# Kernel tuning notes

Hardware: AMD Instinct MI355X
Metric: run time of the kernel (lower is better)

Reference implementation:

```python
import jax, jax.numpy as jnp
import numpy as np

N_EMBD = 1024
N_HEAD = 16
HEAD_DIM = N_EMBD // N_HEAD
SCALE = 1.0 / np.sqrt(HEAD_DIM).astype(np.float32)


def setup_inputs() -> dict:
    key = jax.random.key(0)
    ks = jax.random.split(key, 9)
    B, T = 2, 2048
    std = 1.0 / np.sqrt(N_EMBD).astype(np.float32)
    x = jax.random.normal(ks[0], (B, T, N_EMBD), dtype=jnp.float32)
    Wq = jax.random.normal(ks[1], (N_EMBD, N_EMBD), dtype=jnp.float32) * std
    Wk = jax.random.normal(ks[2], (N_EMBD, N_EMBD), dtype=jnp.float32) * std
    Wv = jax.random.normal(ks[3], (N_EMBD, N_EMBD), dtype=jnp.float32) * std
    Wo = jax.random.normal(ks[4], (N_EMBD, N_EMBD), dtype=jnp.float32) * std
    bq = jax.random.normal(ks[5], (N_EMBD,), dtype=jnp.float32) * 0.01
    bk = jax.random.normal(ks[6], (N_EMBD,), dtype=jnp.float32) * 0.01
    bv = jax.random.normal(ks[7], (N_EMBD,), dtype=jnp.float32) * 0.01
    bo = jax.random.normal(ks[8], (N_EMBD,), dtype=jnp.float32) * 0.01
    return {"x": x, "Wq": Wq, "bq": bq, "Wk": Wk, "bk": bk,
            "Wv": Wv, "bv": bv, "Wo": Wo, "bo": bo}


def reference(x, Wq, bq, Wk, bk, Wv, bv, Wo, bo):
    B, T, C = x.shape
    # project and split heads: (B, H, T, D)
    def heads(y):
        return y.reshape(B, T, N_HEAD, HEAD_DIM).transpose(0, 2, 1, 3)
    q = heads(x @ Wq.T + bq)
    k = heads(x @ Wk.T + bk)
    v = heads(x @ Wv.T + bv)
    # materialized causal attention (matches the torch module's math)
    att = jnp.einsum("bhqd,bhkd->bhqk", q, k) * SCALE
    causal = jnp.tril(jnp.ones((T, T), dtype=bool))
    att = jnp.where(causal, att, -jnp.inf)
    att = jax.nn.softmax(att, axis=-1)
    out = jnp.einsum("bhqk,bhkd->bhqd", att, v)
    out = out.transpose(0, 2, 1, 3).reshape(B, T, C)
    return out @ Wo.T + bo
```

## Files before the change

kernel.cpp:

```cpp
#include <hip/hip_runtime.h>
#include <stdint.h>

typedef unsigned short u16;
typedef __attribute__((ext_vector_type(8))) short short8;
typedef __attribute__((ext_vector_type(4))) float f32x4;

__device__ __forceinline__ u16 f2bf(float f) {
  union { float f; unsigned int u; } c; c.f = f;
  return (u16)((c.u + 0x7FFFu + ((c.u >> 16) & 1u)) >> 16);
}

__device__ __forceinline__ float bf2f(u16 v) {
  union { unsigned int u; float f; } c; c.u = ((unsigned int)v) << 16;
  return c.f;
}

__device__ __forceinline__ f32x4 mfma16(short8 a, short8 b, f32x4 c) {
  return __builtin_amdgcn_mfma_f32_16x16x32_bf16(a, b, c, 0, 0, 0);
}

__device__ __forceinline__ void gl_lds16(const u16* g, u16* l) {
  __builtin_amdgcn_global_load_lds((const __attribute__((address_space(1))) void*)g,
                                   (__attribute__((address_space(3))) void*)l, 16, 0, 0);
}

__global__ __launch_bounds__(256) void cast_all(
    const float* __restrict__ x, const float* __restrict__ wq, const float* __restrict__ wk,
    const float* __restrict__ wv, const float* __restrict__ wo,
    u16* __restrict__ xb, u16* __restrict__ wqb, u16* __restrict__ wkb,
    u16* __restrict__ wvb, u16* __restrict__ wob) {
  int b = blockIdx.x;
  const float* src; u16* dst; int i;
  if (b < 4096)      { src = x;  dst = xb;  i = b * 256 + threadIdx.x; }
  else if (b < 5120) { src = wq; dst = wqb; i = (b - 4096) * 256 + threadIdx.x; }
  else if (b < 6144) { src = wk; dst = wkb; i = (b - 5120) * 256 + threadIdx.x; }
  else if (b < 7168) { src = wv; dst = wvb; i = (b - 6144) * 256 + threadIdx.x; }
  else               { src = wo; dst = wob; i = (b - 7168) * 256 + threadIdx.x; }
  float4 v = ((const float4*)src)[i];
  ushort4 o;
  o.x = f2bf(v.x); o.y = f2bf(v.y); o.z = f2bf(v.z); o.w = f2bf(v.w);
  ((ushort4*)dst)[i] = o;
}

__global__ __launch_bounds__(256) void qkv_gemm(
    const u16* __restrict__ xb, const u16* __restrict__ wqb, const u16* __restrict__ wkb,
    const u16* __restrict__ wvb, const float* __restrict__ bq, const float* __restrict__ bk,
    const float* __restrict__ bv, u16* __restrict__ Qb, u16* __restrict__ Kb,
    u16* __restrict__ VTb) {
  __shared__ __align__(16) u16 As[128 * 32];
  __shared__ __align__(16) u16 Bs[128 * 32];
  const int z = blockIdx.z;
  const u16* __restrict__ W = (z == 0) ? wqb : (z == 1) ? wkb : wvb;
  const float* __restrict__ bias = (z == 0) ? bq : (z == 1) ? bk : bv;
  const int m0 = blockIdx.y * 128, n0 = blockIdx.x * 128;
  const int tid = threadIdx.x, lane = tid & 63, wave = tid >> 6;
  const int wr = (wave >> 1) * 64, wc = (wave & 1) * 64;
  const int fr = lane & 15, fg = lane >> 4;
  const int lrow = lane >> 2, lcol = (lane & 3) * 8;

  const u16* ga = xb + (size_t)(m0 + wave * 16 + lrow) * 1024 + lcol;
  const u16* gb = W  + (size_t)(n0 + wave * 16 + lrow) * 1024 + lcol;
  u16* la = As + wave * 512;
  u16* lb = Bs + wave * 512;

  f32x4 acc[4][4] = {};

  for (int k0 = 0; k0 < 1024; k0 += 32) {
    gl_lds16(ga + k0, la);
    gl_lds16(ga + 64 * 1024 + k0, la + 2048);
    gl_lds16(gb + k0, lb);
    gl_lds16(gb + 64 * 1024 + k0, lb + 2048);
    __syncthreads();
    short8 a[4], b[4];
#pragma unroll
    for (int i = 0; i < 4; ++i) a[i] = *(const short8*)(As + (wr + i * 16 + fr) * 32 + fg * 8);
#pragma unroll
    for (int i = 0; i < 4; ++i) b[i] = *(const short8*)(Bs + (wc + i * 16 + fr) * 32 + fg * 8);
#pragma unroll
    for (int i = 0; i < 4; ++i)
#pragma unroll
      for (int j = 0; j < 4; ++j) acc[i][j] = mfma16(a[i], b[j], acc[i][j]);
    __syncthreads();
  }

  const float qsc = (z == 0) ? (0.125f * 1.44269504088896f) : 1.0f;
#pragma unroll
  for (int j = 0; j < 4; ++j) {
    const int col = n0 + wc + j * 16 + fr;
    const float bcol = bias[col];
    const int h = col >> 6, d = col & 63;
#pragma unroll
    for (int i = 0; i < 4; ++i) {
#pragma unroll
      for (int r = 0; r < 4; ++r) {
        const int m = m0 + wr + i * 16 + fg * 4 + r;
        const int bi = m >> 11, t = m & 2047;
        const u16 o = f2bf((acc[i][j][r] + bcol) * qsc);
        const size_t bse = (size_t)(bi * 16 + h) << 17;
        if (z == 0)      Qb[bse + (size_t)t * 64 + d] = o;
        else if (z == 1) Kb[bse + (size_t)t * 64 + d] = o;
        else             VTb[bse + (size_t)d * 2048 + t] = o;
      }
    }
  }
}

__global__ __launch_bounds__(256, 2) void attn_kernel(
    const u16* __restrict__ Qb, const u16* __restrict__ Kb, const u16* __restrict__ VTb,
    u16* __restrict__ aOb) {
  __shared__ __align__(16) char smem[4 * 64 * 72 * 2];
  __shared__ float Mll[4][4][64];
  u16* Ow = (u16*)smem;
  uint32_t* Pw = (uint32_t*)smem;
  const int id = blockIdx.x;
  const int bh = id & 31, j = 31 - (id >> 5);
  const int tid = threadIdx.x, lane = tid & 63, wave = tid >> 6;
  const int fr = lane & 15, fg = lane >> 4;
  const size_t base = (size_t)bh << 17;
  const int bi = bh >> 4, h = bh & 15;
  const int swz = (fr & 7) << 4;
  const int q0 = j * 64;

  short8 qf[4][2];
#pragma unroll
  for (int mi = 0; mi < 4; ++mi)
#pragma unroll
    for (int kk = 0; kk < 2; ++kk)
      qf[mi][kk] = *(const short8*)(Qb + base +
                    (size_t)(q0 + mi * 16 + fr) * 64 + kk * 32 + fg * 8);

  f32x4 oacc[4][4] = {};
  float lrun[4] = {0.f, 0.f, 0.f, 0.f};

  char* prow = (char*)&Pw[(wave * 16 + fr) * 32];

  for (int ti = wave; ti <= j; ti += 4) {
    const int t0 = ti * 64;
    const u16* kp = Kb + base + (size_t)(t0 + fr) * 64 + fg * 8;
    short8 kf[4][2];
#pragma unroll
    for (int ni = 0; ni < 4; ++ni) {
      kf[ni][0] = *(const short8*)(kp + ni * 1024);
      kf[ni][1] = *(const short8*)(kp + ni * 1024 + 32);
    }
    const u16* vp = VTb + base + (size_t)fr * 2048 + t0 + fg * 8;
    short8 vf[4][2];
#pragma unroll
    for (int ni = 0; ni < 4; ++ni) {
      vf[ni][0] = *(const short8*)(vp + (size_t)ni * 32768);
      vf[ni][1] = *(const short8*)(vp + (size_t)ni * 32768 + 32);
    }

#pragma unroll
    for (int mi = 0; mi < 4; ++mi) {
      f32x4 s[4] = {};
      __builtin_amdgcn_s_setprio(1);
#pragma unroll
      for (int ni = 0; ni < 4; ++ni) {
        s[ni] = mfma16(kf[ni][0], qf[mi][0], s[ni]);
        s[ni] = mfma16(kf[ni][1], qf[mi][1], s[ni]);
      }
      __builtin_amdgcn_s_setprio(0);

      if (ti == j) {
        const int rloc = mi * 16 + fr;
#pragma unroll
        for (int ni = 0; ni < 4; ++ni)
#pragma unroll
          for (int r = 0; r < 4; ++r)
            if (ni * 16 + fg * 4 + r > rloc) s[ni][r] = -1e30f;
      }

      float rs = 0.f;
#pragma unroll
      for (int ni = 0; ni < 4; ++ni)
#pragma unroll
        for (int r = 0; r < 4; ++r) {
          const float pv = exp2f(fminf(s[ni][r], 80.f));
          s[ni][r] = pv;
          rs += pv;
        }
      lrun[mi] += rs;

#pragma unroll
      for (int ni = 0; ni < 4; ++ni) {
        float a0 = s[ni][0], a1 = s[ni][1], a2 = s[ni][2], a3 = s[ni][3];
        uint32_t w0, w1;
        asm("v_cvt_pk_bf16_f32 %0, %1, %2" : "=v"(w0) : "v"(a0), "v"(a1));
        asm("v_cvt_pk_bf16_f32 %0, %1, %2" : "=v"(w1) : "v"(a2), "v"(a3));
        *(uint2*)(prow + ((ni * 32 + fg * 8) ^ swz)) = make_uint2(w0, w1);
      }
      short8 pf[2];
#pragma unroll
      for (int kk = 0; kk < 2; ++kk)
        pf[kk] = *(const short8*)(prow + ((kk * 64 + fg * 16) ^ swz));

      __builtin_amdgcn_s_setprio(1);
#pragma unroll
      for (int ni = 0; ni < 4; ++ni) {
        oacc[mi][ni] = mfma16(pf[0], vf[ni][0], oacc[mi][ni]);
        oacc[mi][ni] = mfma16(pf[1], vf[ni][1], oacc[mi][ni]);
      }
      __builtin_amdgcn_s_setprio(0);
    }
  }

  __syncthreads();
#pragma unroll
  for (int mi = 0; mi < 4; ++mi) Mll[wave][fg][mi * 16 + fr] = lrun[mi];
#pragma unroll
  for (int mi = 0; mi < 4; ++mi)
#pragma unroll
    for (int ni = 0; ni < 4; ++ni)
#pragma unroll
      for (int r = 0; r < 4; ++r)
        Ow[(wave * 64 + mi * 16 + fg * 4 + r) * 72 + ni * 16 + fr] = f2bf(oacc[mi][ni][r]);
  __syncthreads();

  const int rq = tid >> 2, c0 = (tid & 3) * 16;
  float lt = 0.f;
#pragma unroll
  for (int w = 0; w < 4; ++w)
#pragma unroll
    for (int g = 0; g < 4; ++g) lt += Mll[w][g][rq];
  const float inv = __builtin_amdgcn_rcpf(lt);
  float o[16] = {};
#pragma unroll
  for (int w = 0; w < 4; ++w) {
    const u16* orow = &Ow[(w * 64 + rq) * 72 + c0];
    short8 a = *(const short8*)orow;
    short8 b = *(const short8*)(orow + 8);
#pragma unroll
    for (int i = 0; i < 8; ++i) {
      o[i]     += bf2f((u16)a[i]);
      o[8 + i] += bf2f((u16)b[i]);
    }
  }
  short8 r0, r1;
#pragma unroll
  for (int i = 0; i < 8; ++i) {
    r0[i] = (short)f2bf(o[i] * inv);
    r1[i] = (short)f2bf(o[8 + i] * inv);
  }
  u16* op = aOb + ((size_t)bi * 2048 + q0 + rq) * 1024 + h * 64 + c0;
  *(short8*)op = r0;
  *(short8*)(op + 8) = r1;
}

__global__ __launch_bounds__(256) void out_gemm(
    const u16* __restrict__ Ab, const u16* __restrict__ Wb, const float* __restrict__ bo,
    float* __restrict__ out) {
  __shared__ __align__(16) u16 As[128 * 32];
  __shared__ __align__(16) u16 Bs[128 * 32];
  const int m0 = blockIdx.y * 128, n0 = blockIdx.x * 128;
  const int tid = threadIdx.x, lane = tid & 63, wave = tid >> 6;
  const int wr = (wave >> 1) * 64, wc = (wave & 1) * 64;
  const int fr = lane & 15, fg = lane >> 4;
  const int lrow = lane >> 2, lcol = (lane & 3) * 8;

  const u16* ga = Ab + (size_t)(m0 + wave * 16 + lrow) * 1024 + lcol;
  const u16* gb = Wb + (size_t)(n0 + wave * 16 + lrow) * 1024 + lcol;
  u16* la = As + wave * 512;
  u16* lb = Bs + wave * 512;

  f32x4 acc[4][4] = {};

  for (int k0 = 0; k0 < 1024; k0 += 32) {
    gl_lds16(ga + k0, la);
    gl_lds16(ga + 64 * 1024 + k0, la + 2048);
    gl_lds16(gb + k0, lb);
    gl_lds16(gb + 64 * 1024 + k0, lb + 2048);
    __syncthreads();
    short8 a[4], b[4];
#pragma unroll
    for (int i = 0; i < 4; ++i) a[i] = *(const short8*)(As + (wr + i * 16 + fr) * 32 + fg * 8);
#pragma unroll
    for (int i = 0; i < 4; ++i) b[i] = *(const short8*)(Bs + (wc + i * 16 + fr) * 32 + fg * 8);
#pragma unroll
    for (int i = 0; i < 4; ++i)
#pragma unroll
      for (int j = 0; j < 4; ++j) acc[i][j] = mfma16(a[i], b[j], acc[i][j]);
    __syncthreads();
  }

#pragma unroll
  for (int j = 0; j < 4; ++j) {
    const int col = n0 + wc + j * 16 + fr;
    const float bcol = bo[col];
#pragma unroll
    for (int i = 0; i < 4; ++i)
#pragma unroll
      for (int r = 0; r < 4; ++r) {
        const int m = m0 + wr + i * 16 + fg * 4 + r;
        out[(size_t)m * 1024 + col] = acc[i][j][r] + bcol;
      }
  }
}

extern "C" void kernel_launch(void* const* d_in, const int* in_sizes, int n_in,
                              void* d_out, int out_size, void* d_ws, size_t ws_size,
                              hipStream_t stream) {
  (void)in_sizes; (void)n_in; (void)out_size; (void)ws_size;
  const float* x  = (const float*)d_in[0];
  const float* Wq = (const float*)d_in[1];
  const float* bq = (const float*)d_in[2];
  const float* Wk = (const float*)d_in[3];
  const float* bk = (const float*)d_in[4];
  const float* Wv = (const float*)d_in[5];
  const float* bv = (const float*)d_in[6];
  const float* Wo = (const float*)d_in[7];
  const float* bo = (const float*)d_in[8];
  float* out = (float*)d_out;
  char* ws = (char*)d_ws;

  const size_t MB = 1024 * 1024;
  u16* xb  = (u16*)(ws);
  u16* wqb = (u16*)(ws + 8 * MB);
  u16* wkb = (u16*)(ws + 10 * MB);
  u16* wvb = (u16*)(ws + 12 * MB);
  u16* wob = (u16*)(ws + 14 * MB);
  u16* Qb  = (u16*)(ws + 16 * MB);
  u16* Kb  = (u16*)(ws + 24 * MB);
  u16* VTb = (u16*)(ws + 32 * MB);
  u16* aOb = (u16*)(ws + 40 * MB);

  cast_all<<<8192, 256, 0, stream>>>(x, Wq, Wk, Wv, Wo, xb, wqb, wkb, wvb, wob);
  qkv_gemm<<<dim3(8, 32, 3), 256, 0, stream>>>(xb, wqb, wkb, wvb, bq, bk, bv, Qb, Kb, VTb);
  attn_kernel<<<1024, 256, 0, stream>>>(Qb, Kb, VTb, aOb);
  out_gemm<<<dim3(8, 32), 256, 0, stream>>>(aOb, wob, bo, out);
}
```

Baseline: 123.6 us.

## Pair causal query tiles per attention block and swizzle GEMM block order

The attention kernel now works on 32-row query tiles and gives each block two of them, one from the long end of the causal triangle and one from the short end, so every block does about the same amount of work. The aim is to remove the tail imbalance left by the old one-64-row-tile-per-block scheme. Both GEMMs switch to a 1D grid with a grouped tile order, so that consecutive blocks share A and W tiles in cache. The cost is smaller MFMA tiles per wave in attention, K/V reloaded for each pass, and extra syncs.

Result: slower. 143.0 us (+15.7%).

```diff
diff --git a/kernel.cpp b/kernel.cpp
--- a/kernel.cpp
+++ b/kernel.cpp
@@ -49,10 +49,14 @@
     u16* __restrict__ VTb) {
   __shared__ __align__(16) u16 As[128 * 32];
   __shared__ __align__(16) u16 Bs[128 * 32];
-  const int z = blockIdx.z;
+  const int id = blockIdx.x;
+  const int s = id >> 3;
+  const int mblk = (id & 7) + ((s & 3) << 3);
+  const int z = (s >> 2) % 3;
+  const int nblk = s / 12;
   const u16* __restrict__ W = (z == 0) ? wqb : (z == 1) ? wkb : wvb;
   const float* __restrict__ bias = (z == 0) ? bq : (z == 1) ? bk : bv;
-  const int m0 = blockIdx.y * 128, n0 = blockIdx.x * 128;
+  const int m0 = mblk * 128, n0 = nblk * 128;
   const int tid = threadIdx.x, lane = tid & 63, wave = tid >> 6;
   const int wr = (wave >> 1) * 64, wc = (wave & 1) * 64;
   const int fr = lane & 15, fg = lane >> 4;
@@ -108,143 +112,139 @@
 __global__ __launch_bounds__(256, 2) void attn_kernel(
     const u16* __restrict__ Qb, const u16* __restrict__ Kb, const u16* __restrict__ VTb,
     u16* __restrict__ aOb) {
-  __shared__ __align__(16) char smem[4 * 64 * 72 * 2];
-  __shared__ float Mll[4][4][64];
+  __shared__ __align__(16) char smem[4 * 32 * 72 * 2];
+  __shared__ float Mll[4][4][32];
   u16* Ow = (u16*)smem;
   uint32_t* Pw = (uint32_t*)smem;
   const int id = blockIdx.x;
-  const int bh = id & 31, j = 31 - (id >> 5);
+  const int bh = id & 31, p = id >> 5;
   const int tid = threadIdx.x, lane = tid & 63, wave = tid >> 6;
   const int fr = lane & 15, fg = lane >> 4;
   const size_t base = (size_t)bh << 17;
   const int bi = bh >> 4, h = bh & 15;
   const int swz = (fr & 7) << 4;
-  const int q0 = j * 64;
-
-  short8 qf[4][2];
-#pragma unroll
-  for (int mi = 0; mi < 4; ++mi)
-#pragma unroll
-    for (int kk = 0; kk < 2; ++kk)
-      qf[mi][kk] = *(const short8*)(Qb + base +
-                    (size_t)(q0 + mi * 16 + fr) * 64 + kk * 32 + fg * 8);
-
-  f32x4 oacc[4][4] = {};
-  float lrun[4] = {0.f, 0.f, 0.f, 0.f};
-
   char* prow = (char*)&Pw[(wave * 16 + fr) * 32];
 
-  for (int ti = wave; ti <= j; ti += 4) {
-    const int t0 = ti * 64;
-    const u16* kp = Kb + base + (size_t)(t0 + fr) * 64 + fg * 8;
-    short8 kf[4][2];
-#pragma unroll
-    for (int ni = 0; ni < 4; ++ni) {
-      kf[ni][0] = *(const short8*)(kp + ni * 1024);
-      kf[ni][1] = *(const short8*)(kp + ni * 1024 + 32);
+#pragma unroll
+  for (int pass = 0; pass < 2; ++pass) {
+    const int jj = pass ? p : (63 - p);
+    const int q0 = jj * 32;
+    const int nt = (jj >> 1) + 1;
+
+    short8 qf[2][2];
+#pragma unroll
+    for (int mi = 0; mi < 2; ++mi)
+#pragma unroll
+      for (int kk = 0; kk < 2; ++kk)
+        qf[mi][kk] = *(const short8*)(Qb + base +
+                      (size_t)(q0 + mi * 16 + fr) * 64 + kk * 32 + fg * 8);
+
+    f32x4 oacc[2][4] = {};
+    float lrun[2] = {0.f, 0.f};
+
+    for (int ti = wave; ti < nt; ti += 4) {
+      const int t0 = ti * 64;
+      const u16* kp = Kb + base + (size_t)(t0 + fr) * 64 + fg * 8;
+      short8 kf[4][2];
+#pragma unroll
+      for (int ni = 0; ni < 4; ++ni) {
+        kf[ni][0] = *(const short8*)(kp + ni * 1024);
+        kf[ni][1] = *(const short8*)(kp + ni * 1024 + 32);
+      }
+      const u16* vp = VTb + base + (size_t)fr * 2048 + t0 + fg * 8;
+      short8 vf[4][2];
+#pragma unroll
+      for (int ni = 0; ni < 4; ++ni) {
+        vf[ni][0] = *(const short8*)(vp + (size_t)ni * 32768);
+        vf[ni][1] = *(const short8*)(vp + (size_t)ni * 32768 + 32);
+      }
+
+#pragma unroll
+      for (int mi = 0; mi < 2; ++mi) {
+        f32x4 s[4] = {};
+        __builtin_amdgcn_s_setprio(1);
+#pragma unroll
+        for (int ni = 0; ni < 4; ++ni) {
+          s[ni] = mfma16(kf[ni][0], qf[mi][0], s[ni]);
+          s[ni] = mfma16(kf[ni][1], qf[mi][1], s[ni]);
+        }
+        __builtin_amdgcn_s_setprio(0);
+
+        if (ti == nt - 1) {
+          const int rlim = (mi * 16 + fr) + (q0 - t0);
+#pragma unroll
+          for (int ni = 0; ni < 4; ++ni)
+#pragma unroll
+            for (int r = 0; r < 4; ++r)
+              if (ni * 16 + fg * 4 + r > rlim) s[ni][r] = -1e30f;
+        }
+
+        float rs = 0.f;
+#pragma unroll
+        for (int ni = 0; ni < 4; ++ni)
+#pragma unroll
+          for (int r = 0; r < 4; ++r) {
+            const float pv = exp2f(fminf(s[ni][r], 80.f));
+            s[ni][r] = pv;
+            rs += pv;
+          }
+        lrun[mi] += rs;
+
+#pragma unroll
+        for (int ni = 0; ni < 4; ++ni) {
+          float a0 = s[ni][0], a1 = s[ni][1], a2 = s[ni][2], a3 = s[ni][3];
+          uint32_t w0, w1;
+          asm("v_cvt_pk_bf16_f32 %0, %1, %2" : "=v"(w0) : "v"(a0), "v"(a1));
+          asm("v_cvt_pk_bf16_f32 %0, %1, %2" : "=v"(w1) : "v"(a2), "v"(a3));
+          *(uint2*)(prow + ((ni * 32 + fg * 8) ^ swz)) = make_uint2(w0, w1);
+        }
+        short8 pf[2];
+#pragma unroll
+        for (int kk = 0; kk < 2; ++kk)
+          pf[kk] = *(const short8*)(prow + ((kk * 64 + fg * 16) ^ swz));
+
+        __builtin_amdgcn_s_setprio(1);
+#pragma unroll
+        for (int ni = 0; ni < 4; ++ni) {
+          oacc[mi][ni] = mfma16(pf[0], vf[ni][0], oacc[mi][ni]);
+          oacc[mi][ni] = mfma16(pf[1], vf[ni][1], oacc[mi][ni]);
+        }
+        __builtin_amdgcn_s_setprio(0);
+      }
     }
-    const u16* vp = VTb + base + (size_t)fr * 2048 + t0 + fg * 8;
-    short8 vf[4][2];
-#pragma unroll
-    for (int ni = 0; ni < 4; ++ni) {
-      vf[ni][0] = *(const short8*)(vp + (size_t)ni * 32768);
-      vf[ni][1] = *(const short8*)(vp + (size_t)ni * 32768 + 32);
+
+    __syncthreads();
+#pragma unroll
+    for (int mi = 0; mi < 2; ++mi) Mll[wave][fg][mi * 16 + fr] = lrun[mi];
+#pragma unroll
+    for (int mi = 0; mi < 2; ++mi)
+#pragma unroll
+      for (int ni = 0; ni < 4; ++ni)
+#pragma unroll
+        for (int r = 0; r < 4; ++r)
+          Ow[(wave * 32 + mi * 16 + fg * 4 + r) * 72 + ni * 16 + fr] = f2bf(oacc[mi][ni][r]);
+    __syncthreads();
+
+    const int rq = tid >> 3, c0 = (tid & 7) * 8;
+    float lt = 0.f;
+#pragma unroll
+    for (int w = 0; w < 4; ++w)
+#pragma unroll
+      for (int g = 0; g < 4; ++g) lt += Mll[w][g][rq];
+    const float inv = __builtin_amdgcn_rcpf(lt);
+    float o[8] = {};
+#pragma unroll
+    for (int w = 0; w < 4; ++w) {
+      short8 a = *(const short8*)&Ow[(w * 32 + rq) * 72 + c0];
+#pragma unroll
+      for (int i = 0; i < 8; ++i) o[i] += bf2f((u16)a[i]);
     }
-
-#pragma unroll
-    for (int mi = 0; mi < 4; ++mi) {
-      f32x4 s[4] = {};
-      __builtin_amdgcn_s_setprio(1);
-#pragma unroll
-      for (int ni = 0; ni < 4; ++ni) {
-        s[ni] = mfma16(kf[ni][0], qf[mi][0], s[ni]);
-        s[ni] = mfma16(kf[ni][1], qf[mi][1], s[ni]);
-      }
-      __builtin_amdgcn_s_setprio(0);
-
-      if (ti == j) {
-        const int rloc = mi * 16 + fr;
-#pragma unroll
-        for (int ni = 0; ni < 4; ++ni)
-#pragma unroll
-          for (int r = 0; r < 4; ++r)
-            if (ni * 16 + fg * 4 + r > rloc) s[ni][r] = -1e30f;
-      }
-
-      float rs = 0.f;
-#pragma unroll
-      for (int ni = 0; ni < 4; ++ni)
-#pragma unroll
-        for (int r = 0; r < 4; ++r) {
-          const float pv = exp2f(fminf(s[ni][r], 80.f));
-          s[ni][r] = pv;
-          rs += pv;
-        }
-      lrun[mi] += rs;
-
-#pragma unroll
-      for (int ni = 0; ni < 4; ++ni) {
-        float a0 = s[ni][0], a1 = s[ni][1], a2 = s[ni][2], a3 = s[ni][3];
-        uint32_t w0, w1;
-        asm("v_cvt_pk_bf16_f32 %0, %1, %2" : "=v"(w0) : "v"(a0), "v"(a1));
-        asm("v_cvt_pk_bf16_f32 %0, %1, %2" : "=v"(w1) : "v"(a2), "v"(a3));
-        *(uint2*)(prow + ((ni * 32 + fg * 8) ^ swz)) = make_uint2(w0, w1);
-      }
-      short8 pf[2];
-#pragma unroll
-      for (int kk = 0; kk < 2; ++kk)
-        pf[kk] = *(const short8*)(prow + ((kk * 64 + fg * 16) ^ swz));
-
-      __builtin_amdgcn_s_setprio(1);
-#pragma unroll
-      for (int ni = 0; ni < 4; ++ni) {
-        oacc[mi][ni] = mfma16(pf[0], vf[ni][0], oacc[mi][ni]);
-        oacc[mi][ni] = mfma16(pf[1], vf[ni][1], oacc[mi][ni]);
-      }
-      __builtin_amdgcn_s_setprio(0);
-    }
-  }
-
-  __syncthreads();
-#pragma unroll
-  for (int mi = 0; mi < 4; ++mi) Mll[wave][fg][mi * 16 + fr] = lrun[mi];
-#pragma unroll
-  for (int mi = 0; mi < 4; ++mi)
-#pragma unroll
-    for (int ni = 0; ni < 4; ++ni)
-#pragma unroll
-      for (int r = 0; r < 4; ++r)
-        Ow[(wave * 64 + mi * 16 + fg * 4 + r) * 72 + ni * 16 + fr] = f2bf(oacc[mi][ni][r]);
-  __syncthreads();
-
-  const int rq = tid >> 2, c0 = (tid & 3) * 16;
-  float lt = 0.f;
-#pragma unroll
-  for (int w = 0; w < 4; ++w)
-#pragma unroll
-    for (int g = 0; g < 4; ++g) lt += Mll[w][g][rq];
-  const float inv = __builtin_amdgcn_rcpf(lt);
-  float o[16] = {};
-#pragma unroll
-  for (int w = 0; w < 4; ++w) {
-    const u16* orow = &Ow[(w * 64 + rq) * 72 + c0];
-    short8 a = *(const short8*)orow;
-    short8 b = *(const short8*)(orow + 8);
-#pragma unroll
-    for (int i = 0; i < 8; ++i) {
-      o[i]     += bf2f((u16)a[i]);
-      o[8 + i] += bf2f((u16)b[i]);
-    }
-  }
-  short8 r0, r1;
-#pragma unroll
-  for (int i = 0; i < 8; ++i) {
-    r0[i] = (short)f2bf(o[i] * inv);
-    r1[i] = (short)f2bf(o[8 + i] * inv);
-  }
-  u16* op = aOb + ((size_t)bi * 2048 + q0 + rq) * 1024 + h * 64 + c0;
-  *(short8*)op = r0;
-  *(short8*)(op + 8) = r1;
+    short8 r0;
+#pragma unroll
+    for (int i = 0; i < 8; ++i) r0[i] = (short)f2bf(o[i] * inv);
+    *(short8*)(aOb + ((size_t)bi * 2048 + q0 + rq) * 1024 + h * 64 + c0) = r0;
+    __syncthreads();
+  }
 }
 
 __global__ __launch_bounds__(256) void out_gemm(
@@ -252,7 +252,10 @@
     float* __restrict__ out) {
   __shared__ __align__(16) u16 As[128 * 32];
   __shared__ __align__(16) u16 Bs[128 * 32];
-  const int m0 = blockIdx.y * 128, n0 = blockIdx.x * 128;
+  const int id = blockIdx.x;
+  const int s = id >> 3;
+  const int m0 = ((id & 7) + ((s & 3) << 3)) * 128;
+  const int n0 = (s >> 2) * 128;
   const int tid = threadIdx.x, lane = tid & 63, wave = tid >> 6;
   const int wr = (wave >> 1) * 64, wc = (wave & 1) * 64;
   const int fr = lane & 15, fg = lane >> 4;
@@ -325,7 +328,7 @@
   u16* aOb = (u16*)(ws + 40 * MB);
 
   cast_all<<<8192, 256, 0, stream>>>(x, Wq, Wk, Wv, Wo, xb, wqb, wkb, wvb, wob);
-  qkv_gemm<<<dim3(8, 32, 3), 256, 0, stream>>>(xb, wqb, wkb, wvb, bq, bk, bv, Qb, Kb, VTb);
+  qkv_gemm<<<768, 256, 0, stream>>>(xb, wqb, wkb, wvb, bq, bk, bv, Qb, Kb, VTb);
   attn_kernel<<<1024, 256, 0, stream>>>(Qb, Kb, VTb, aOb);
-  out_gemm<<<dim3(8, 32), 256, 0, stream>>>(aOb, wob, bo, out);
-}
+  out_gemm<<<256, 256, 0, stream>>>(aOb, wob, bo, out);
+}
```

## Split long causal attention rows into KV chunks with merge kernel; remap GEMM block order

Applied to the files above, without the earlier changes.

Attention work for later query tiles is split into up to four 512-key chunks computed by separate blocks. Each chunk writes unnormalized partial outputs and row sums, and a new merge kernel combines them. This balances the causal workload across more blocks (2560 instead of 1024) at the cost of an extra launch and partial-buffer traffic. The QKV and output GEMMs also switch to a 1D grid with a swizzled block order for better cache locality, and the workspace layout is reshuffled so some buffers alias.

New measurement: 136.9 us. 1.11x slower.

```diff
diff --git a/kernel.cpp b/kernel.cpp
--- a/kernel.cpp
+++ b/kernel.cpp
@@ -49,10 +49,14 @@
     u16* __restrict__ VTb) {
   __shared__ __align__(16) u16 As[128 * 32];
   __shared__ __align__(16) u16 Bs[128 * 32];
-  const int z = blockIdx.z;
+  const int id = blockIdx.x;
+  const int s = id >> 3;
+  const int mblk = (id & 7) + ((s & 3) << 3);
+  const int z = (s >> 2) % 3;
+  const int nblk = s / 12;
   const u16* __restrict__ W = (z == 0) ? wqb : (z == 1) ? wkb : wvb;
   const float* __restrict__ bias = (z == 0) ? bq : (z == 1) ? bk : bv;
-  const int m0 = blockIdx.y * 128, n0 = blockIdx.x * 128;
+  const int m0 = mblk * 128, n0 = nblk * 128;
   const int tid = threadIdx.x, lane = tid & 63, wave = tid >> 6;
   const int wr = (wave >> 1) * 64, wc = (wave & 1) * 64;
   const int fr = lane & 15, fg = lane >> 4;
@@ -107,19 +111,25 @@
 
 __global__ __launch_bounds__(256, 2) void attn_kernel(
     const u16* __restrict__ Qb, const u16* __restrict__ Kb, const u16* __restrict__ VTb,
-    u16* __restrict__ aOb) {
+    u16* __restrict__ Opart, float* __restrict__ Lpart, u16* __restrict__ aOb) {
   __shared__ __align__(16) char smem[4 * 64 * 72 * 2];
   __shared__ float Mll[4][4][64];
   u16* Ow = (u16*)smem;
   uint32_t* Pw = (uint32_t*)smem;
   const int id = blockIdx.x;
-  const int bh = id & 31, j = 31 - (id >> 5);
+  const int bh = id & 31, r = id >> 5;
+  int j, c;
+  if (r < 8)       { j = r;                  c = 0; }
+  else if (r < 24) { j = 8 + ((r - 8) >> 1); c = (r - 8) & 1; }
+  else if (r < 48) { j = 16 + (r - 24) / 3;  c = (r - 24) % 3; }
+  else             { j = 24 + ((r - 48) >> 2); c = (r - 48) & 3; }
   const int tid = threadIdx.x, lane = tid & 63, wave = tid >> 6;
   const int fr = lane & 15, fg = lane >> 4;
   const size_t base = (size_t)bh << 17;
   const int bi = bh >> 4, h = bh & 15;
   const int swz = (fr & 7) << 4;
   const int q0 = j * 64;
+  char* prow = (char*)&Pw[(wave * 16 + fr) * 32];
 
   short8 qf[4][2];
 #pragma unroll
@@ -132,9 +142,8 @@
   f32x4 oacc[4][4] = {};
   float lrun[4] = {0.f, 0.f, 0.f, 0.f};
 
-  char* prow = (char*)&Pw[(wave * 16 + fr) * 32];
-
-  for (int ti = wave; ti <= j; ti += 4) {
+  const int thi = min(c * 8 + 7, j);
+  for (int ti = c * 8 + wave; ti <= thi; ti += 4) {
     const int t0 = ti * 64;
     const u16* kp = Kb + base + (size_t)(t0 + fr) * 64 + fg * 8;
     short8 kf[4][2];
@@ -167,17 +176,17 @@
 #pragma unroll
         for (int ni = 0; ni < 4; ++ni)
 #pragma unroll
-          for (int r = 0; r < 4; ++r)
-            if (ni * 16 + fg * 4 + r > rloc) s[ni][r] = -1e30f;
+          for (int rr = 0; rr < 4; ++rr)
+            if (ni * 16 + fg * 4 + rr > rloc) s[ni][rr] = -1e30f;
       }
 
       float rs = 0.f;
 #pragma unroll
       for (int ni = 0; ni < 4; ++ni)
 #pragma unroll
-        for (int r = 0; r < 4; ++r) {
-          const float pv = exp2f(fminf(s[ni][r], 80.f));
-          s[ni][r] = pv;
+        for (int rr = 0; rr < 4; ++rr) {
+          const float pv = exp2f(fminf(s[ni][rr], 80.f));
+          s[ni][rr] = pv;
           rs += pv;
         }
       lrun[mi] += rs;
@@ -213,8 +222,8 @@
 #pragma unroll
     for (int ni = 0; ni < 4; ++ni)
 #pragma unroll
-      for (int r = 0; r < 4; ++r)
-        Ow[(wave * 64 + mi * 16 + fg * 4 + r) * 72 + ni * 16 + fr] = f2bf(oacc[mi][ni][r]);
+      for (int rr = 0; rr < 4; ++rr)
+        Ow[(wave * 64 + mi * 16 + fg * 4 + rr) * 72 + ni * 16 + fr] = f2bf(oacc[mi][ni][rr]);
   __syncthreads();
 
   const int rq = tid >> 2, c0 = (tid & 3) * 16;
@@ -223,7 +232,6 @@
   for (int w = 0; w < 4; ++w)
 #pragma unroll
     for (int g = 0; g < 4; ++g) lt += Mll[w][g][rq];
-  const float inv = __builtin_amdgcn_rcpf(lt);
   float o[16] = {};
 #pragma unroll
   for (int w = 0; w < 4; ++w) {
@@ -236,13 +244,65 @@
       o[8 + i] += bf2f((u16)b[i]);
     }
   }
+  if (j < 8) {
+    const float inv = __builtin_amdgcn_rcpf(lt);
+    short8 r0, r1;
+#pragma unroll
+    for (int i = 0; i < 8; ++i) {
+      r0[i] = (short)f2bf(o[i] * inv);
+      r1[i] = (short)f2bf(o[8 + i] * inv);
+    }
+    u16* op = aOb + ((size_t)bi * 2048 + q0 + rq) * 1024 + h * 64 + c0;
+    *(short8*)op = r0;
+    *(short8*)(op + 8) = r1;
+  } else {
+    short8 r0, r1;
+#pragma unroll
+    for (int i = 0; i < 8; ++i) {
+      r0[i] = (short)f2bf(o[i]);
+      r1[i] = (short)f2bf(o[8 + i]);
+    }
+    u16* op = Opart + (size_t)id * 4096 + rq * 64 + c0;
+    *(short8*)op = r0;
+    *(short8*)(op + 8) = r1;
+    if ((tid & 3) == 0) Lpart[id * 64 + rq] = lt;
+  }
+}
+
+__global__ __launch_bounds__(256) void attn_merge(
+    const u16* __restrict__ Opart, const float* __restrict__ Lpart,
+    u16* __restrict__ aOb) {
+  const int id = blockIdx.x;
+  const int bh = id & 31, j = 8 + (id >> 5);
+  const int nc = (j >> 3) + 1;
+  const int tid = threadIdx.x;
+  const int rq = tid >> 2, c0 = (tid & 3) * 16;
+  const int bi = bh >> 4, h = bh & 15;
+  float o[16] = {};
+  float lt = 0.f;
+  for (int cc = 0; cc < nc; ++cc) {
+    const int rr = (j < 16) ? 8 + ((j - 8) << 1) + cc
+                 : (j < 24) ? 24 + 3 * (j - 16) + cc
+                            : 48 + ((j - 24) << 2) + cc;
+    const int slot = (rr << 5) | bh;
+    lt += Lpart[slot * 64 + rq];
+    const u16* op = Opart + (size_t)slot * 4096 + rq * 64 + c0;
+    short8 a = *(const short8*)op;
+    short8 b = *(const short8*)(op + 8);
+#pragma unroll
+    for (int i = 0; i < 8; ++i) {
+      o[i]     += bf2f((u16)a[i]);
+      o[8 + i] += bf2f((u16)b[i]);
+    }
+  }
+  const float inv = __builtin_amdgcn_rcpf(lt);
   short8 r0, r1;
 #pragma unroll
   for (int i = 0; i < 8; ++i) {
     r0[i] = (short)f2bf(o[i] * inv);
     r1[i] = (short)f2bf(o[8 + i] * inv);
   }
-  u16* op = aOb + ((size_t)bi * 2048 + q0 + rq) * 1024 + h * 64 + c0;
+  u16* op = aOb + ((size_t)bi * 2048 + j * 64 + rq) * 1024 + h * 64 + c0;
   *(short8*)op = r0;
   *(short8*)(op + 8) = r1;
 }
@@ -252,7 +312,10 @@
     float* __restrict__ out) {
   __shared__ __align__(16) u16 As[128 * 32];
   __shared__ __align__(16) u16 Bs[128 * 32];
-  const int m0 = blockIdx.y * 128, n0 = blockIdx.x * 128;
+  const int id = blockIdx.x;
+  const int s = id >> 3;
+  const int m0 = ((id & 7) + ((s & 3) << 3)) * 128;
+  const int n0 = (s >> 2) * 128;
   const int tid = threadIdx.x, lane = tid & 63, wave = tid >> 6;
   const int wr = (wave >> 1) * 64, wc = (wave & 1) * 64;
   const int fr = lane & 15, fg = lane >> 4;
@@ -314,18 +377,21 @@
   char* ws = (char*)d_ws;
 
   const size_t MB = 1024 * 1024;
-  u16* xb  = (u16*)(ws);
-  u16* wqb = (u16*)(ws + 8 * MB);
-  u16* wkb = (u16*)(ws + 10 * MB);
-  u16* wvb = (u16*)(ws + 12 * MB);
-  u16* wob = (u16*)(ws + 14 * MB);
-  u16* Qb  = (u16*)(ws + 16 * MB);
-  u16* Kb  = (u16*)(ws + 24 * MB);
-  u16* VTb = (u16*)(ws + 32 * MB);
-  u16* aOb = (u16*)(ws + 40 * MB);
+  u16*   wob   = (u16*)(ws);
+  u16*   xb    = (u16*)(ws + 2 * MB);
+  u16*   aOb   = (u16*)(ws + 2 * MB);
+  u16*   wqb   = (u16*)(ws + 10 * MB);
+  float* Lpart = (float*)(ws + 10 * MB);
+  u16*   wkb   = (u16*)(ws + 12 * MB);
+  u16*   wvb   = (u16*)(ws + 14 * MB);
+  u16*   Qb    = (u16*)(ws + 16 * MB);
+  u16*   Kb    = (u16*)(ws + 24 * MB);
+  u16*   VTb   = (u16*)(ws + 32 * MB);
+  u16*   Opart = (u16*)(ws + 40 * MB);
 
   cast_all<<<8192, 256, 0, stream>>>(x, Wq, Wk, Wv, Wo, xb, wqb, wkb, wvb, wob);
-  qkv_gemm<<<dim3(8, 32, 3), 256, 0, stream>>>(xb, wqb, wkb, wvb, bq, bk, bv, Qb, Kb, VTb);
-  attn_kernel<<<1024, 256, 0, stream>>>(Qb, Kb, VTb, aOb);
-  out_gemm<<<dim3(8, 32), 256, 0, stream>>>(aOb, wob, bo, out);
-}
+  qkv_gemm<<<768, 256, 0, stream>>>(xb, wqb, wkb, wvb, bq, bk, bv, Qb, Kb, VTb);
+  attn_kernel<<<2560, 256, 0, stream>>>(Qb, Kb, VTb, Opart, Lpart, aOb);
+  attn_merge<<<768, 256, 0, stream>>>(Opart, Lpart, aOb);
+  out_gemm<<<256, 256, 0, stream>>>(aOb, wob, bo, out);
+}
```

## Switch attention to 32x32 MFMA with permlane P reuse and remap GEMM grids

Applied to the files above, without the earlier changes.

Rewrites the attention inner loop to use 32x32x16 bf16 MFMA tiles. P now goes straight from the score accumulator into the PV MFMA operand through v_permlane32_swap, so the round trip through LDS is gone. It also drops the fminf clamp before exp2f, which removes overflow protection on large logits. Separately, the QKV and output GEMMs move to a 1D grid with a block remapping that groups M tiles, aiming at better L2 locality for weights and activations across XCDs.

Result: faster. 117.3 us (-5.1%).

```diff
diff --git a/kernel.cpp b/kernel.cpp
--- a/kernel.cpp
+++ b/kernel.cpp
@@ -4,6 +4,7 @@
 typedef unsigned short u16;
 typedef __attribute__((ext_vector_type(8))) short short8;
 typedef __attribute__((ext_vector_type(4))) float f32x4;
+typedef __attribute__((ext_vector_type(16))) float f32x16;
 
 __device__ __forceinline__ u16 f2bf(float f) {
   union { float f; unsigned int u; } c; c.f = f;
@@ -17,6 +18,10 @@
 
 __device__ __forceinline__ f32x4 mfma16(short8 a, short8 b, f32x4 c) {
   return __builtin_amdgcn_mfma_f32_16x16x32_bf16(a, b, c, 0, 0, 0);
+}
+
+__device__ __forceinline__ f32x16 mfma32(short8 a, short8 b, f32x16 c) {
+  return __builtin_amdgcn_mfma_f32_32x32x16_bf16(a, b, c, 0, 0, 0);
 }
 
 __device__ __forceinline__ void gl_lds16(const u16* g, u16* l) {
@@ -49,10 +54,14 @@
     u16* __restrict__ VTb) {
   __shared__ __align__(16) u16 As[128 * 32];
   __shared__ __align__(16) u16 Bs[128 * 32];
-  const int z = blockIdx.z;
+  const int id = blockIdx.x;
+  const int s = id >> 3;
+  const int mblk = (id & 7) + ((s & 3) << 3);
+  const int z = (s >> 2) % 3;
+  const int nblk = s / 12;
   const u16* __restrict__ W = (z == 0) ? wqb : (z == 1) ? wkb : wvb;
   const float* __restrict__ bias = (z == 0) ? bq : (z == 1) ? bk : bv;
-  const int m0 = blockIdx.y * 128, n0 = blockIdx.x * 128;
+  const int m0 = mblk * 128, n0 = nblk * 128;
   const int tid = threadIdx.x, lane = tid & 63, wave = tid >> 6;
   const int wr = (wave >> 1) * 64, wc = (wave & 1) * 64;
   const int fr = lane & 15, fg = lane >> 4;
@@ -108,113 +117,121 @@
 __global__ __launch_bounds__(256, 2) void attn_kernel(
     const u16* __restrict__ Qb, const u16* __restrict__ Kb, const u16* __restrict__ VTb,
     u16* __restrict__ aOb) {
-  __shared__ __align__(16) char smem[4 * 64 * 72 * 2];
-  __shared__ float Mll[4][4][64];
-  u16* Ow = (u16*)smem;
-  uint32_t* Pw = (uint32_t*)smem;
+  __shared__ __align__(16) u16 Ow[4 * 64 * 72];
+  __shared__ float Mll[4][2][64];
   const int id = blockIdx.x;
   const int bh = id & 31, j = 31 - (id >> 5);
   const int tid = threadIdx.x, lane = tid & 63, wave = tid >> 6;
-  const int fr = lane & 15, fg = lane >> 4;
+  const int l31 = lane & 31, hi = lane >> 5;
   const size_t base = (size_t)bh << 17;
   const int bi = bh >> 4, h = bh & 15;
-  const int swz = (fr & 7) << 4;
   const int q0 = j * 64;
 
-  short8 qf[4][2];
-#pragma unroll
-  for (int mi = 0; mi < 4; ++mi)
-#pragma unroll
-    for (int kk = 0; kk < 2; ++kk)
-      qf[mi][kk] = *(const short8*)(Qb + base +
-                    (size_t)(q0 + mi * 16 + fr) * 64 + kk * 32 + fg * 8);
-
-  f32x4 oacc[4][4] = {};
-  float lrun[4] = {0.f, 0.f, 0.f, 0.f};
-
-  char* prow = (char*)&Pw[(wave * 16 + fr) * 32];
+  short8 qf[2][4];
+  {
+    const u16* qp = Qb + base + (size_t)(q0 + l31) * 64 + hi * 8;
+#pragma unroll
+    for (int mi = 0; mi < 2; ++mi)
+#pragma unroll
+      for (int st = 0; st < 4; ++st)
+        qf[mi][st] = *(const short8*)(qp + mi * 32 * 64 + st * 16);
+  }
+
+  f32x16 oacc[2][2] = {};
+  float lrun[2] = {0.f, 0.f};
 
   for (int ti = wave; ti <= j; ti += 4) {
     const int t0 = ti * 64;
-    const u16* kp = Kb + base + (size_t)(t0 + fr) * 64 + fg * 8;
-    short8 kf[4][2];
-#pragma unroll
-    for (int ni = 0; ni < 4; ++ni) {
-      kf[ni][0] = *(const short8*)(kp + ni * 1024);
-      kf[ni][1] = *(const short8*)(kp + ni * 1024 + 32);
-    }
-    const u16* vp = VTb + base + (size_t)fr * 2048 + t0 + fg * 8;
-    short8 vf[4][2];
-#pragma unroll
-    for (int ni = 0; ni < 4; ++ni) {
-      vf[ni][0] = *(const short8*)(vp + (size_t)ni * 32768);
-      vf[ni][1] = *(const short8*)(vp + (size_t)ni * 32768 + 32);
-    }
-
-#pragma unroll
-    for (int mi = 0; mi < 4; ++mi) {
-      f32x4 s[4] = {};
-      __builtin_amdgcn_s_setprio(1);
-#pragma unroll
-      for (int ni = 0; ni < 4; ++ni) {
-        s[ni] = mfma16(kf[ni][0], qf[mi][0], s[ni]);
-        s[ni] = mfma16(kf[ni][1], qf[mi][1], s[ni]);
-      }
-      __builtin_amdgcn_s_setprio(0);
-
-      if (ti == j) {
-        const int rloc = mi * 16 + fr;
-#pragma unroll
-        for (int ni = 0; ni < 4; ++ni)
-#pragma unroll
-          for (int r = 0; r < 4; ++r)
-            if (ni * 16 + fg * 4 + r > rloc) s[ni][r] = -1e30f;
-      }
-
-      float rs = 0.f;
-#pragma unroll
-      for (int ni = 0; ni < 4; ++ni)
-#pragma unroll
-        for (int r = 0; r < 4; ++r) {
-          const float pv = exp2f(fminf(s[ni][r], 80.f));
-          s[ni][r] = pv;
+    const u16* kp = Kb + base + (size_t)(t0 + l31) * 64 + hi * 8;
+    short8 kf[2][4];
+#pragma unroll
+    for (int tb = 0; tb < 2; ++tb)
+#pragma unroll
+      for (int st = 0; st < 4; ++st)
+        kf[tb][st] = *(const short8*)(kp + tb * 32 * 64 + st * 16);
+    const u16* vp = VTb + base + (size_t)l31 * 2048 + t0 + hi * 8;
+    short8 vf[2][2][2];
+#pragma unroll
+    for (int nb = 0; nb < 2; ++nb)
+#pragma unroll
+      for (int tb = 0; tb < 2; ++tb)
+#pragma unroll
+        for (int ks = 0; ks < 2; ++ks)
+          vf[nb][tb][ks] = *(const short8*)(vp + (size_t)nb * 32 * 2048 + tb * 32 + ks * 16);
+
+#pragma unroll
+    for (int mi = 0; mi < 2; ++mi) {
+#pragma unroll
+      for (int tb = 0; tb < 2; ++tb) {
+        f32x16 s = {};
+        __builtin_amdgcn_s_setprio(1);
+        s = mfma32(kf[tb][0], qf[mi][0], s);
+        s = mfma32(kf[tb][1], qf[mi][1], s);
+        s = mfma32(kf[tb][2], qf[mi][2], s);
+        s = mfma32(kf[tb][3], qf[mi][3], s);
+        __builtin_amdgcn_s_setprio(0);
+
+        if (ti == j) {
+          const int qv = mi * 32 + l31;
+          const int tbb = tb * 32 + hi * 4;
+#pragma unroll
+          for (int r = 0; r < 16; ++r) {
+            const int tl = tbb + (r & 3) + ((r >> 2) << 3);
+            if (tl > qv) s[r] = -1e30f;
+          }
+        }
+
+        float rs = 0.f;
+#pragma unroll
+        for (int r = 0; r < 16; ++r) {
+          const float pv = exp2f(s[r]);
+          s[r] = pv;
           rs += pv;
         }
-      lrun[mi] += rs;
-
-#pragma unroll
-      for (int ni = 0; ni < 4; ++ni) {
-        float a0 = s[ni][0], a1 = s[ni][1], a2 = s[ni][2], a3 = s[ni][3];
-        uint32_t w0, w1;
-        asm("v_cvt_pk_bf16_f32 %0, %1, %2" : "=v"(w0) : "v"(a0), "v"(a1));
-        asm("v_cvt_pk_bf16_f32 %0, %1, %2" : "=v"(w1) : "v"(a2), "v"(a3));
-        *(uint2*)(prow + ((ni * 32 + fg * 8) ^ swz)) = make_uint2(w0, w1);
+        lrun[mi] += rs;
+
+        uint32_t w0, w1, w2, w3, w4, w5, w6, w7;
+        asm("v_cvt_pk_bf16_f32 %0, %1, %2" : "=v"(w0) : "v"(s[0]),  "v"(s[1]));
+        asm("v_cvt_pk_bf16_f32 %0, %1, %2" : "=v"(w1) : "v"(s[2]),  "v"(s[3]));
+        asm("v_cvt_pk_bf16_f32 %0, %1, %2" : "=v"(w2) : "v"(s[4]),  "v"(s[5]));
+        asm("v_cvt_pk_bf16_f32 %0, %1, %2" : "=v"(w3) : "v"(s[6]),  "v"(s[7]));
+        asm("v_cvt_pk_bf16_f32 %0, %1, %2" : "=v"(w4) : "v"(s[8]),  "v"(s[9]));
+        asm("v_cvt_pk_bf16_f32 %0, %1, %2" : "=v"(w5) : "v"(s[10]), "v"(s[11]));
+        asm("v_cvt_pk_bf16_f32 %0, %1, %2" : "=v"(w6) : "v"(s[12]), "v"(s[13]));
+        asm("v_cvt_pk_bf16_f32 %0, %1, %2" : "=v"(w7) : "v"(s[14]), "v"(s[15]));
+        asm("v_permlane32_swap_b32 %0, %1" : "+v"(w0), "+v"(w2));
+        asm("v_permlane32_swap_b32 %0, %1" : "+v"(w1), "+v"(w3));
+        asm("v_permlane32_swap_b32 %0, %1" : "+v"(w4), "+v"(w6));
+        asm("v_permlane32_swap_b32 %0, %1" : "+v"(w5), "+v"(w7));
+        short8 pa0, pa1;
+        {
+          uint32_t* p0 = (uint32_t*)&pa0;
+          p0[0] = w0; p0[1] = w1; p0[2] = w2; p0[3] = w3;
+          uint32_t* p1 = (uint32_t*)&pa1;
+          p1[0] = w4; p1[1] = w5; p1[2] = w6; p1[3] = w7;
+        }
+
+        __builtin_amdgcn_s_setprio(1);
+        oacc[mi][0] = mfma32(pa0, vf[0][tb][0], oacc[mi][0]);
+        oacc[mi][0] = mfma32(pa1, vf[0][tb][1], oacc[mi][0]);
+        oacc[mi][1] = mfma32(pa0, vf[1][tb][0], oacc[mi][1]);
+        oacc[mi][1] = mfma32(pa1, vf[1][tb][1], oacc[mi][1]);
+        __builtin_amdgcn_s_setprio(0);
       }
-      short8 pf[2];
-#pragma unroll
-      for (int kk = 0; kk < 2; ++kk)
-        pf[kk] = *(const short8*)(prow + ((kk * 64 + fg * 16) ^ swz));
-
-      __builtin_amdgcn_s_setprio(1);
-#pragma unroll
-      for (int ni = 0; ni < 4; ++ni) {
-        oacc[mi][ni] = mfma16(pf[0], vf[ni][0], oacc[mi][ni]);
-        oacc[mi][ni] = mfma16(pf[1], vf[ni][1], oacc[mi][ni]);
+    }
+  }
+
+#pragma unroll
+  for (int mi = 0; mi < 2; ++mi) Mll[wave][hi][mi * 32 + l31] = lrun[mi];
+#pragma unroll
+  for (int mi = 0; mi < 2; ++mi)
+#pragma unroll
+    for (int nb = 0; nb < 2; ++nb)
+#pragma unroll
+      for (int r = 0; r < 16; ++r) {
+        const int q = mi * 32 + (r & 3) + ((r >> 2) << 3) + hi * 4;
+        Ow[(wave * 64 + q) * 72 + nb * 32 + l31] = f2bf(oacc[mi][nb][r]);
       }
-      __builtin_amdgcn_s_setprio(0);
-    }
-  }
-
-  __syncthreads();
-#pragma unroll
-  for (int mi = 0; mi < 4; ++mi) Mll[wave][fg][mi * 16 + fr] = lrun[mi];
-#pragma unroll
-  for (int mi = 0; mi < 4; ++mi)
-#pragma unroll
-    for (int ni = 0; ni < 4; ++ni)
-#pragma unroll
-      for (int r = 0; r < 4; ++r)
-        Ow[(wave * 64 + mi * 16 + fg * 4 + r) * 72 + ni * 16 + fr] = f2bf(oacc[mi][ni][r]);
   __syncthreads();
 
   const int rq = tid >> 2, c0 = (tid & 3) * 16;
@@ -222,7 +239,7 @@
 #pragma unroll
   for (int w = 0; w < 4; ++w)
 #pragma unroll
-    for (int g = 0; g < 4; ++g) lt += Mll[w][g][rq];
+    for (int g = 0; g < 2; ++g) lt += Mll[w][g][rq];
   const float inv = __builtin_amdgcn_rcpf(lt);
   float o[16] = {};
 #pragma unroll
@@ -252,7 +269,10 @@
     float* __restrict__ out) {
   __shared__ __align__(16) u16 As[128 * 32];
   __shared__ __align__(16) u16 Bs[128 * 32];
-  const int m0 = blockIdx.y * 128, n0 = blockIdx.x * 128;
+  const int id = blockIdx.x;
+  const int s = id >> 3;
+  const int m0 = ((id & 7) + ((s & 3) << 3)) * 128;
+  const int n0 = (s >> 2) * 128;
   const int tid = threadIdx.x, lane = tid & 63, wave = tid >> 6;
   const int wr = (wave >> 1) * 64, wc = (wave & 1) * 64;
   const int fr = lane & 15, fg = lane >> 4;
@@ -325,7 +345,7 @@
   u16* aOb = (u16*)(ws + 40 * MB);
 
   cast_all<<<8192, 256, 0, stream>>>(x, Wq, Wk, Wv, Wo, xb, wqb, wkb, wvb, wob);
-  qkv_gemm<<<dim3(8, 32, 3), 256, 0, stream>>>(xb, wqb, wkb, wvb, bq, bk, bv, Qb, Kb, VTb);
+  qkv_gemm<<<768, 256, 0, stream>>>(xb, wqb, wkb, wvb, bq, bk, bv, Qb, Kb, VTb);
   attn_kernel<<<1024, 256, 0, stream>>>(Qb, Kb, VTb, aOb);
-  out_gemm<<<dim3(8, 32), 256, 0, stream>>>(aOb, wob, bo, out);
-}
+  out_gemm<<<256, 256, 0, stream>>>(aOb, wob, bo, out);
+}
```
